# Optimization experiments

Hardware: AMD Instinct MI355X
Metric: run time of the kernel (lower is better)

## Reference

```python
import jax, jax.numpy as jnp
import numpy as np

B, T, H, DH = 4, 2048, 16, 128
D = H * DH            # inner_dim = 2048
F = 4096              # mlp_inner_dim
E = 8                 # num_expert_mlp
TOP_K = 2


def setup_inputs() -> dict:
    key = jax.random.key(0)
    ks = jax.random.split(key, 5)
    s_in = 1.0 / np.sqrt(D)
    s_f = 1.0 / np.sqrt(F)
    return {
        "stm": jax.random.normal(ks[0], (B, T, H, DH), dtype=jnp.float32),
        "gate_w": jax.random.normal(ks[1], (E, D), dtype=jnp.float32) * s_in,
        "w1": jax.random.normal(ks[2], (E, F, D), dtype=jnp.float32) * s_in,
        "w2": jax.random.normal(ks[3], (E, D, F), dtype=jnp.float32) * s_f,
        "w3": jax.random.normal(ks[4], (E, F, D), dtype=jnp.float32) * s_in,
    }


def reference(stm, gate_w, w1, w2, w3):
    b, t, h, dh = stm.shape
    d = h * dh
    x = stm.reshape(b * t, d)                                   # [N, D]
    logits = x @ gate_w.T                                       # [N, E]
    top_logit, top_idx = jax.lax.top_k(logits, TOP_K)           # [N, 2]
    gw = jax.nn.softmax(top_logit.astype(jnp.float32), axis=1).astype(x.dtype)
    out = jnp.zeros_like(x)
    n_expert = w1.shape[0]
    for e in range(n_expert):
        # combine weight for expert e per token (0 if not routed)
        we = jnp.sum(jnp.where(top_idx == e, gw, jnp.zeros_like(gw)), axis=1)  # [N]
        gate = jax.nn.silu(x @ w1[e].T)                          # [N, F]
        up = x @ w3[e].T                                         # [N, F]
        y = (gate * up) @ w2[e].T                                # [N, D]
        out = out + we[:, None] * y
    return out.reshape(b, t, h, dh)
```

## Files before the change

kernel.cpp:

```cpp
#include <hip/hip_runtime.h>
#include <hip/hip_bf16.h>
#include <stdint.h>

#define N_TOK 8192
#define DIM   2048
#define FDIM  4096
#define NEXP  8

#define XB_OFF   0ull
#define HB_OFF   33554432ull
#define WB1_OFF  176160768ull
#define WB3_OFF  243269632ull
#define META_OFF 310378496ull
#define CNT_OFF   (META_OFF)
#define EBASE_OFF (META_OFF + 64ull)
#define ELIST_OFF (META_OFF + 128ull)
#define EWTS_OFF  (ELIST_OFF + 262144ull)

typedef float f32x4 __attribute__((ext_vector_type(4)));
typedef short s16x8 __attribute__((ext_vector_type(8)));

__device__ __forceinline__ uint32_t pkbf(float a, float b) {
  uint32_t ua = __builtin_bit_cast(uint32_t, a) + 0x8000u;
  uint32_t ub = __builtin_bit_cast(uint32_t, b) + 0x8000u;
  return (ua >> 16) | (ub & 0xffff0000u);
}

__device__ __forceinline__ void gld16(const void* g, void* l) {
  __builtin_amdgcn_global_load_lds(
      (__attribute__((address_space(1))) void*)g,
      (__attribute__((address_space(3))) void*)l, 16, 0, 0);
}

__device__ __forceinline__ void conv_chunks(
    const float* __restrict__ src, __hip_bfloat16* __restrict__ dst,
    int r0, int nrh, int rtot, int kd, int idx0, int stride, int total) {
  const int cpr = kd / 8;
  for (int i = idx0; i < total; i += stride) {
    const int e = i / (nrh * cpr);
    const int rem = i - e * nrh * cpr;
    const int lr = rem / cpr;
    const int c = rem - lr * cpr;
    const float* s = src + ((size_t)e * rtot + r0 + lr) * (size_t)kd + c * 8;
    const float4 a = *(const float4*)s;
    const float4 b = *(const float4*)(s + 4);
    uint4 u;
    u.x = pkbf(a.x, a.y); u.y = pkbf(a.z, a.w);
    u.z = pkbf(b.x, b.y); u.w = pkbf(b.z, b.w);
    *(uint4*)(dst + ((size_t)e * nrh + lr) * (size_t)kd + c * 8) = u;
  }
}

__global__ void init_k(int* cnt) {
  if (threadIdx.x < NEXP) cnt[threadIdx.x] = 0;
}

__global__ void router_k(const float* __restrict__ x, const float* __restrict__ gw,
                         __hip_bfloat16* __restrict__ xb, int* __restrict__ cnt,
                         int* __restrict__ elist, float* __restrict__ ewts,
                         const float* __restrict__ w1, const float* __restrict__ w3,
                         __hip_bfloat16* __restrict__ wA, __hip_bfloat16* __restrict__ wB,
                         float* __restrict__ out) {
  const int blk = blockIdx.x;
  const int t = threadIdx.x;
  if (blk >= N_TOK) {
    const int cb = blk - N_TOK;
    if (cb < 4096) {
      conv_chunks(w1, wA, 0, 2048, FDIM, DIM, cb * 256 + t, 4096 * 256, 4194304);
    } else if (cb < 8192) {
      conv_chunks(w3, wB, 0, 2048, FDIM, DIM, (cb - 4096) * 256 + t, 4096 * 256, 4194304);
    } else {
      for (size_t i = (size_t)(cb - 8192) * 256 + t; i < 4194304; i += 512 * 256)
        *(float4*)(out + i * 4) = make_float4(0.f, 0.f, 0.f, 0.f);
    }
    return;
  }
  const int n = blk;
  const float* xr = x + (size_t)n * DIM;
  const float4 v0 = *(const float4*)(xr + t * 8);
  const float4 v1 = *(const float4*)(xr + t * 8 + 4);
  uint4 u;
  u.x = pkbf(v0.x, v0.y); u.y = pkbf(v0.z, v0.w);
  u.z = pkbf(v1.x, v1.y); u.w = pkbf(v1.z, v1.w);
  *(uint4*)(xb + (size_t)n * DIM + t * 8) = u;

  float p[NEXP];
#pragma unroll
  for (int e = 0; e < NEXP; ++e) {
    const float* g = gw + e * DIM + t * 8;
    const float4 g0 = *(const float4*)g;
    const float4 g1 = *(const float4*)(g + 4);
    p[e] = v0.x * g0.x + v0.y * g0.y + v0.z * g0.z + v0.w * g0.w +
           v1.x * g1.x + v1.y * g1.y + v1.z * g1.z + v1.w * g1.w;
  }
#pragma unroll
  for (int off = 32; off >= 1; off >>= 1)
#pragma unroll
    for (int e = 0; e < NEXP; ++e) p[e] += __shfl_xor(p[e], off, 64);

  __shared__ float red[4][NEXP];
  const int lane = t & 63, wv = t >> 6;
  if (lane == 0) {
#pragma unroll
    for (int e = 0; e < NEXP; ++e) red[wv][e] = p[e];
  }
  __syncthreads();
  if (t == 0) {
    float l0 = -1e30f, l1 = -1e30f;
    int e0 = 0, e1 = 0;
#pragma unroll
    for (int e = 0; e < NEXP; ++e) {
      float v = red[0][e] + red[1][e] + red[2][e] + red[3][e];
      if (v > l0) { l1 = l0; e1 = e0; l0 = v; e0 = e; }
      else if (v > l1) { l1 = v; e1 = e; }
    }
    const float ed = expf(l1 - l0);
    const float inv = 1.f / (1.f + ed);
    int s0 = atomicAdd(cnt + e0, 1);
    elist[e0 * N_TOK + s0] = n;
    ewts[e0 * N_TOK + s0] = inv;
    int s1 = atomicAdd(cnt + e1, 1);
    elist[e1 * N_TOK + s1] = (int)((uint32_t)n | 0x80000000u);
    ewts[e1 * N_TOK + s1] = ed * inv;
  }
}

__global__ void scan_k(const int* __restrict__ cnt, int* __restrict__ ebase) {
  if (threadIdx.x == 0 && blockIdx.x == 0) {
    int b = 0;
    for (int e = 0; e < NEXP; ++e) { ebase[e] = b; b += (cnt[e] + 127) & ~127; }
  }
}

__global__ void convH_k(const float* __restrict__ w1, __hip_bfloat16* __restrict__ d1,
                        const float* __restrict__ w3, __hip_bfloat16* __restrict__ d3,
                        int r0) {
  const int idx0 = blockIdx.x * 256 + threadIdx.x;
  conv_chunks(w1, d1, r0, 2048, FDIM, DIM, idx0, 4096 * 256, 4194304);
  conv_chunks(w3, d3, r0, 2048, FDIM, DIM, idx0, 4096 * 256, 4194304);
}

__global__ void convW_k(const float* __restrict__ src, __hip_bfloat16* __restrict__ dst,
                        int r0, int nrh, int rtot, int kd) {
  conv_chunks(src, dst, r0, nrh, rtot, kd,
              blockIdx.x * blockDim.x + threadIdx.x, gridDim.x * blockDim.x,
              NEXP * nrh * (kd / 8));
}

__global__ __launch_bounds__(256, 2) void moe_up_k(
    const __hip_bfloat16* __restrict__ xb, const __hip_bfloat16* __restrict__ w1b,
    const __hip_bfloat16* __restrict__ w3b, __hip_bfloat16* __restrict__ hb,
    const int* __restrict__ cnt, const int* __restrict__ ebase,
    const int* __restrict__ elist, int noff) {
  constexpr int NT = DIM / 32;
  const int e = blockIdx.z;
  const int count = cnt[e];
  const int mt = blockIdx.y;
  if (mt * 128 >= count) return;
  const int bn0 = blockIdx.x * 128;
  const int ncol0 = noff + bn0;

  __shared__ char lds[73728];
  const int t = threadIdx.x;
  const int lane = t & 63, wv = t >> 6;
  const int wr = wv >> 1, wc = wv & 1;
  const int* lst = elist + e * N_TOK;
  const size_t hrow0 = (size_t)ebase[e] + (size_t)mt * 128;

  const int r0 = t >> 2;
  const int ks = (t & 3) ^ ((r0 >> 1) & 3);
  size_t sA[2], sB1[2];
  int ldsO[2];
#pragma unroll
  for (int i = 0; i < 2; ++i) {
    const int r = r0 + i * 64;
    int idx = mt * 128 + r;
    if (idx >= count) idx = 0;
    const size_t tok = (size_t)(lst[idx] & 0x7fffffff);
    sA[i] = tok * DIM + ks * 8;
    sB1[i] = ((size_t)e * 2048 + bn0 + r) * DIM + ks * 8;
    ldsO[i] = i * 4096 + wv * 1024;
  }

  const int fr = lane & 15;
  const int swzc = ((lane >> 4) ^ ((fr >> 1) & 3)) << 4;
  const int aoff = (wr * 64 + fr) * 64 + swzc;
  const int boff = (wc * 64 + fr) * 64 + swzc;

  f32x4 accG[4][4], accU[4][4];
#pragma unroll
  for (int mi = 0; mi < 4; ++mi)
#pragma unroll
    for (int ni = 0; ni < 4; ++ni) {
      accG[mi][ni] = {0.f, 0.f, 0.f, 0.f};
      accU[mi][ni] = {0.f, 0.f, 0.f, 0.f};
    }

  auto stage = [&](int kt, int b) {
    const int k0 = kt * 32;
    char* base = lds + b * 24576;
#pragma unroll
    for (int i = 0; i < 2; ++i)
      gld16(xb + sA[i] + k0, base + ldsO[i]);
#pragma unroll
    for (int i = 0; i < 2; ++i)
      gld16(w1b + sB1[i] + k0, base + 8192 + ldsO[i]);
#pragma unroll
    for (int i = 0; i < 2; ++i)
      gld16(w3b + sB1[i] + k0, base + 16384 + ldsO[i]);
  };

  stage(0, 0);
  stage(1, 1);
  asm volatile("s_waitcnt vmcnt(6)" ::: "memory");
  __builtin_amdgcn_sched_barrier(0);
  __builtin_amdgcn_s_barrier();
  __builtin_amdgcn_sched_barrier(0);

  int bR = 0, bS = 2;
#pragma unroll 3
  for (int kt = 0; kt < NT; ++kt) {
    const int t2 = (kt + 2 < NT) ? kt + 2 : NT - 1;
    stage(t2, bS);
    char* base = lds + bR * 24576;
    s16x8 af[4], b1f[4], b3f[4];
#pragma unroll
    for (int mi = 0; mi < 4; ++mi)
      af[mi] = *(const s16x8*)(base + aoff + mi * 1024);
#pragma unroll
    for (int ni = 0; ni < 4; ++ni) {
      b1f[ni] = *(const s16x8*)(base + 8192 + boff + ni * 1024);
      b3f[ni] = *(const s16x8*)(base + 16384 + boff + ni * 1024);
    }
#pragma unroll
    for (int mi = 0; mi < 4; ++mi)
#pragma unroll
      for (int ni = 0; ni < 4; ++ni) {
        accG[mi][ni] = __builtin_amdgcn_mfma_f32_16x16x32_bf16(
            af[mi], b1f[ni], accG[mi][ni], 0, 0, 0);
        accU[mi][ni] = __builtin_amdgcn_mfma_f32_16x16x32_bf16(
            af[mi], b3f[ni], accU[mi][ni], 0, 0, 0);
      }
    asm volatile("s_waitcnt vmcnt(6)" ::: "memory");
    __builtin_amdgcn_sched_barrier(0);
    __builtin_amdgcn_s_barrier();
    __builtin_amdgcn_sched_barrier(0);
    bR = (bR == 2) ? 0 : bR + 1;
    bS = (bS == 2) ? 0 : bS + 1;
  }

  const int erow = (lane >> 4) * 4;
  const int ecol = lane & 15;
#pragma unroll
  for (int mi = 0; mi < 4; ++mi)
#pragma unroll
    for (int ni = 0; ni < 4; ++ni) {
      const size_t cb = ncol0 + wc * 64 + ni * 16 + ecol;
#pragma unroll
      for (int j = 0; j < 4; ++j) {
        const size_t r = hrow0 + wr * 64 + mi * 16 + erow + j;
        const float g = accG[mi][ni][j];
        const float uu = accU[mi][ni][j];
        const float h = g / (1.f + __expf(-g)) * uu;
        hb[r * FDIM + cb] = __float2bfloat16(h);
      }
    }
}

__global__ __launch_bounds__(256, 2) void moe_down_k(
    const __hip_bfloat16* __restrict__ hb, const __hip_bfloat16* __restrict__ w2b,
    float* __restrict__ out, const int* __restrict__ cnt,
    const int* __restrict__ ebase, const int* __restrict__ elist,
    const float* __restrict__ ewts) {
  constexpr int NT = FDIM / 32;
  const int e = blockIdx.z;
  const int count = cnt[e];
  const int mt = blockIdx.y;
  if (mt * 128 >= count) return;
  const int bn0 = blockIdx.x * 256;

  __shared__ char lds[73728];
  const int t = threadIdx.x;
  const int lane = t & 63, wv = t >> 6;
  const int wr = wv >> 1, wc = wv & 1;
  const int* lst = elist + e * N_TOK;
  const size_t hrow0 = (size_t)ebase[e] + (size_t)mt * 128;

  const int r0 = t >> 2;
  const int ks = (t & 3) ^ ((r0 >> 1) & 3);
  size_t sA[2], sB[2];
  int ldsO[2];
#pragma unroll
  for (int i = 0; i < 2; ++i) {
    const int r = r0 + i * 64;
    sA[i] = (hrow0 + r) * (size_t)FDIM + ks * 8;
    sB[i] = ((size_t)e * 2048 + bn0 + r) * (size_t)FDIM + ks * 8;
    ldsO[i] = i * 4096 + wv * 1024;
  }
  const size_t sBp = 128 * (size_t)FDIM;

  const int fr = lane & 15;
  const int swzc = ((lane >> 4) ^ ((fr >> 1) & 3)) << 4;
  const int aoff = (wr * 64 + fr) * 64 + swzc;
  const int boff = (wc * 64 + fr) * 64 + swzc;

  f32x4 accP[2][4][4];
#pragma unroll
  for (int p = 0; p < 2; ++p)
#pragma unroll
    for (int mi = 0; mi < 4; ++mi)
#pragma unroll
      for (int ni = 0; ni < 4; ++ni) accP[p][mi][ni] = {0.f, 0.f, 0.f, 0.f};

  auto stage = [&](int kt, int b) {
    const int k0 = kt * 32;
    char* base = lds + b * 24576;
#pragma unroll
    for (int i = 0; i < 2; ++i)
      gld16(hb + sA[i] + k0, base + ldsO[i]);
#pragma unroll
    for (int i = 0; i < 2; ++i)
      gld16(w2b + sB[i] + k0, base + 8192 + ldsO[i]);
#pragma unroll
    for (int i = 0; i < 2; ++i)
      gld16(w2b + sB[i] + sBp + k0, base + 16384 + ldsO[i]);
  };

  stage(0, 0);
  stage(1, 1);
  asm volatile("s_waitcnt vmcnt(6)" ::: "memory");
  __builtin_amdgcn_sched_barrier(0);
  __builtin_amdgcn_s_barrier();
  __builtin_amdgcn_sched_barrier(0);

  int bR = 0, bS = 2;
#pragma unroll 3
  for (int kt = 0; kt < NT; ++kt) {
    const int t2 = (kt + 2 < NT) ? kt + 2 : NT - 1;
    stage(t2, bS);
    char* base = lds + bR * 24576;
    s16x8 af[4], b0f[4], b1f[4];
#pragma unroll
    for (int mi = 0; mi < 4; ++mi)
      af[mi] = *(const s16x8*)(base + aoff + mi * 1024);
#pragma unroll
    for (int ni = 0; ni < 4; ++ni) {
      b0f[ni] = *(const s16x8*)(base + 8192 + boff + ni * 1024);
      b1f[ni] = *(const s16x8*)(base + 16384 + boff + ni * 1024);
    }
#pragma unroll
    for (int mi = 0; mi < 4; ++mi)
#pragma unroll
      for (int ni = 0; ni < 4; ++ni) {
        accP[0][mi][ni] = __builtin_amdgcn_mfma_f32_16x16x32_bf16(
            af[mi], b0f[ni], accP[0][mi][ni], 0, 0, 0);
        accP[1][mi][ni] = __builtin_amdgcn_mfma_f32_16x16x32_bf16(
            af[mi], b1f[ni], accP[1][mi][ni], 0, 0, 0);
      }
    asm volatile("s_waitcnt vmcnt(6)" ::: "memory");
    __builtin_amdgcn_sched_barrier(0);
    __builtin_amdgcn_s_barrier();
    __builtin_amdgcn_sched_barrier(0);
    bR = (bR == 2) ? 0 : bR + 1;
    bS = (bS == 2) ? 0 : bS + 1;
  }

  const int erow = (lane >> 4) * 4;
  const int ecol = lane & 15;
#pragma unroll
  for (int mi = 0; mi < 4; ++mi)
#pragma unroll
    for (int j = 0; j < 4; ++j) {
      const int i = mt * 128 + wr * 64 + mi * 16 + erow + j;
      if (i < count) {
        const uint32_t info = (uint32_t)lst[i];
        const int tok = (int)(info & 0x7fffffffu);
        const float wt = ewts[e * N_TOK + i];
        float* prow = out + (size_t)tok * DIM;
#pragma unroll
        for (int p = 0; p < 2; ++p)
#pragma unroll
          for (int ni = 0; ni < 4; ++ni) {
            const int cb = bn0 + p * 128 + wc * 64 + ni * 16 + ecol;
            atomicAdd(prow + cb, wt * accP[p][mi][ni][j]);
          }
      }
    }
}

extern "C" void kernel_launch(void* const* d_in, const int* in_sizes, int n_in,
                              void* d_out, int out_size, void* d_ws, size_t ws_size,
                              hipStream_t stream) {
  const float* stm = (const float*)d_in[0];
  const float* gw = (const float*)d_in[1];
  const float* w1 = (const float*)d_in[2];
  const float* w2 = (const float*)d_in[3];
  const float* w3 = (const float*)d_in[4];
  float* out = (float*)d_out;
  char* ws = (char*)d_ws;

  __hip_bfloat16* xb = (__hip_bfloat16*)(ws + XB_OFF);
  __hip_bfloat16* hb = (__hip_bfloat16*)(ws + HB_OFF);
  __hip_bfloat16* wb1 = (__hip_bfloat16*)(ws + WB1_OFF);
  __hip_bfloat16* wb3 = (__hip_bfloat16*)(ws + WB3_OFF);
  __hip_bfloat16* w2full = (__hip_bfloat16*)(ws + WB1_OFF);
  int* cnt = (int*)(ws + CNT_OFF);
  int* ebase = (int*)(ws + EBASE_OFF);
  int* elist = (int*)(ws + ELIST_OFF);
  float* ewts = (float*)(ws + EWTS_OFF);

  init_k<<<1, 64, 0, stream>>>(cnt);
  router_k<<<N_TOK + 8704, 256, 0, stream>>>(stm, gw, xb, cnt, elist, ewts,
                                             w1, w3, wb1, wb3, out);
  scan_k<<<1, 64, 0, stream>>>(cnt, ebase);

  const dim3 gUp(16, 64, 8);
  const dim3 gDn(8, 64, 8);

  moe_up_k<<<gUp, 256, 0, stream>>>(xb, wb1, wb3, hb, cnt, ebase, elist, 0);

  convH_k<<<4096, 256, 0, stream>>>(w1, wb1, w3, wb3, 2048);
  moe_up_k<<<gUp, 256, 0, stream>>>(xb, wb1, wb3, hb, cnt, ebase, elist, 2048);

  convW_k<<<4096, 256, 0, stream>>>(w2, w2full, 0, 2048, DIM, FDIM);
  moe_down_k<<<gDn, 256, 0, stream>>>(hb, w2full, out, cnt, ebase, elist, ewts);
}
```

Before: 1.350 ms.

## Enlarge MoE GEMM tiles to 256 rows with 512-thread, 8-wave blocks

Both expert GEMM kernels move from 256-thread blocks with 128-row M tiles to 512-thread blocks with 256-row M tiles. Expert segments are padded to 256 rows to match. In the up kernel the 8 waves share one B tile, and the down kernel now uses a 4x2 wave grid over a 256x256 output tile with 8x4 accumulators per wave. The aim is to halve weight re-reads per token and raise arithmetic intensity. The cost is fewer resident blocks, more padding waste per expert and higher register pressure in the down kernel.

Result: slower. 1.408 ms (+4.3%).

```diff
diff --git a/kernel.cpp b/kernel.cpp
--- a/kernel.cpp
+++ b/kernel.cpp
@@ -128,7 +128,7 @@
 __global__ void scan_k(const int* __restrict__ cnt, int* __restrict__ ebase) {
   if (threadIdx.x == 0 && blockIdx.x == 0) {
     int b = 0;
-    for (int e = 0; e < NEXP; ++e) { ebase[e] = b; b += (cnt[e] + 127) & ~127; }
+    for (int e = 0; e < NEXP; ++e) { ebase[e] = b; b += (cnt[e] + 255) & ~255; }
   }
 }
 
@@ -147,7 +147,7 @@
               NEXP * nrh * (kd / 8));
 }
 
-__global__ __launch_bounds__(256, 2) void moe_up_k(
+__global__ __launch_bounds__(512, 1) void moe_up_k(
     const __hip_bfloat16* __restrict__ xb, const __hip_bfloat16* __restrict__ w1b,
     const __hip_bfloat16* __restrict__ w3b, __hip_bfloat16* __restrict__ hb,
     const int* __restrict__ cnt, const int* __restrict__ ebase,
@@ -156,36 +156,39 @@
   const int e = blockIdx.z;
   const int count = cnt[e];
   const int mt = blockIdx.y;
-  if (mt * 128 >= count) return;
+  if (mt * 256 >= count) return;
   const int bn0 = blockIdx.x * 128;
   const int ncol0 = noff + bn0;
 
-  __shared__ char lds[73728];
+  __shared__ char lds[98304];
   const int t = threadIdx.x;
   const int lane = t & 63, wv = t >> 6;
   const int wr = wv >> 1, wc = wv & 1;
   const int* lst = elist + e * N_TOK;
-  const size_t hrow0 = (size_t)ebase[e] + (size_t)mt * 128;
-
-  const int r0 = t >> 2;
-  const int ks = (t & 3) ^ ((r0 >> 1) & 3);
-  size_t sA[2], sB1[2];
-  int ldsO[2];
+  const size_t hrow0 = (size_t)ebase[e] + (size_t)mt * 256;
+
+  const int sl = t & 3;
+  size_t sA[2];
+  int ldsA[2];
 #pragma unroll
   for (int i = 0; i < 2; ++i) {
-    const int r = r0 + i * 64;
-    int idx = mt * 128 + r;
+    const int row = (t >> 2) + i * 128;
+    const int gsrc = sl ^ ((row >> 1) & 3);
+    int idx = mt * 256 + row;
     if (idx >= count) idx = 0;
     const size_t tok = (size_t)(lst[idx] & 0x7fffffff);
-    sA[i] = tok * DIM + ks * 8;
-    sB1[i] = ((size_t)e * 2048 + bn0 + r) * DIM + ks * 8;
-    ldsO[i] = i * 4096 + wv * 1024;
-  }
+    sA[i] = tok * DIM + gsrc * 8;
+    ldsA[i] = wv * 1024 + i * 8192;
+  }
+  const int rB = t >> 2;
+  const int gsrcB = sl ^ ((rB >> 1) & 3);
+  const size_t sB = ((size_t)e * 2048 + bn0 + rB) * DIM + gsrcB * 8;
+  const int ldsB = 16384 + wv * 1024;
 
   const int fr = lane & 15;
   const int swzc = ((lane >> 4) ^ ((fr >> 1) & 3)) << 4;
   const int aoff = (wr * 64 + fr) * 64 + swzc;
-  const int boff = (wc * 64 + fr) * 64 + swzc;
+  const int boff = 16384 + (wc * 64 + fr) * 64 + swzc;
 
   f32x4 accG[4][4], accU[4][4];
 #pragma unroll
@@ -198,21 +201,17 @@
 
   auto stage = [&](int kt, int b) {
     const int k0 = kt * 32;
-    char* base = lds + b * 24576;
+    char* base = lds + b * 32768;
 #pragma unroll
     for (int i = 0; i < 2; ++i)
-      gld16(xb + sA[i] + k0, base + ldsO[i]);
-#pragma unroll
-    for (int i = 0; i < 2; ++i)
-      gld16(w1b + sB1[i] + k0, base + 8192 + ldsO[i]);
-#pragma unroll
-    for (int i = 0; i < 2; ++i)
-      gld16(w3b + sB1[i] + k0, base + 16384 + ldsO[i]);
+      gld16(xb + sA[i] + k0, base + ldsA[i]);
+    gld16(w1b + sB + k0, base + ldsB);
+    gld16(w3b + sB + k0, base + ldsB + 8192);
   };
 
   stage(0, 0);
   stage(1, 1);
-  asm volatile("s_waitcnt vmcnt(6)" ::: "memory");
+  asm volatile("s_waitcnt vmcnt(4)" ::: "memory");
   __builtin_amdgcn_sched_barrier(0);
   __builtin_amdgcn_s_barrier();
   __builtin_amdgcn_sched_barrier(0);
@@ -222,15 +221,15 @@
   for (int kt = 0; kt < NT; ++kt) {
     const int t2 = (kt + 2 < NT) ? kt + 2 : NT - 1;
     stage(t2, bS);
-    char* base = lds + bR * 24576;
+    char* base = lds + bR * 32768;
     s16x8 af[4], b1f[4], b3f[4];
 #pragma unroll
     for (int mi = 0; mi < 4; ++mi)
       af[mi] = *(const s16x8*)(base + aoff + mi * 1024);
 #pragma unroll
     for (int ni = 0; ni < 4; ++ni) {
-      b1f[ni] = *(const s16x8*)(base + 8192 + boff + ni * 1024);
-      b3f[ni] = *(const s16x8*)(base + 16384 + boff + ni * 1024);
+      b1f[ni] = *(const s16x8*)(base + boff + ni * 1024);
+      b3f[ni] = *(const s16x8*)(base + boff + 8192 + ni * 1024);
     }
 #pragma unroll
     for (int mi = 0; mi < 4; ++mi)
@@ -241,7 +240,7 @@
         accU[mi][ni] = __builtin_amdgcn_mfma_f32_16x16x32_bf16(
             af[mi], b3f[ni], accU[mi][ni], 0, 0, 0);
       }
-    asm volatile("s_waitcnt vmcnt(6)" ::: "memory");
+    asm volatile("s_waitcnt vmcnt(4)" ::: "memory");
     __builtin_amdgcn_sched_barrier(0);
     __builtin_amdgcn_s_barrier();
     __builtin_amdgcn_sched_barrier(0);
@@ -267,7 +266,7 @@
     }
 }
 
-__global__ __launch_bounds__(256, 2) void moe_down_k(
+__global__ __launch_bounds__(512, 1) void moe_down_k(
     const __hip_bfloat16* __restrict__ hb, const __hip_bfloat16* __restrict__ w2b,
     float* __restrict__ out, const int* __restrict__ cnt,
     const int* __restrict__ ebase, const int* __restrict__ elist,
@@ -276,59 +275,53 @@
   const int e = blockIdx.z;
   const int count = cnt[e];
   const int mt = blockIdx.y;
-  if (mt * 128 >= count) return;
+  if (mt * 256 >= count) return;
   const int bn0 = blockIdx.x * 256;
 
-  __shared__ char lds[73728];
+  __shared__ char lds[98304];
   const int t = threadIdx.x;
   const int lane = t & 63, wv = t >> 6;
-  const int wr = wv >> 1, wc = wv & 1;
+  const int wr = wv >> 2, wc = wv & 3;
   const int* lst = elist + e * N_TOK;
-  const size_t hrow0 = (size_t)ebase[e] + (size_t)mt * 128;
-
-  const int r0 = t >> 2;
-  const int ks = (t & 3) ^ ((r0 >> 1) & 3);
+  const size_t hrow0 = (size_t)ebase[e] + (size_t)mt * 256;
+
+  const int sl = t & 3;
   size_t sA[2], sB[2];
   int ldsO[2];
 #pragma unroll
   for (int i = 0; i < 2; ++i) {
-    const int r = r0 + i * 64;
-    sA[i] = (hrow0 + r) * (size_t)FDIM + ks * 8;
-    sB[i] = ((size_t)e * 2048 + bn0 + r) * (size_t)FDIM + ks * 8;
-    ldsO[i] = i * 4096 + wv * 1024;
-  }
-  const size_t sBp = 128 * (size_t)FDIM;
+    const int row = (t >> 2) + i * 128;
+    const int gsrc = sl ^ ((row >> 1) & 3);
+    sA[i] = (hrow0 + row) * (size_t)FDIM + gsrc * 8;
+    sB[i] = ((size_t)e * 2048 + bn0 + row) * (size_t)FDIM + gsrc * 8;
+    ldsO[i] = wv * 1024 + i * 8192;
+  }
 
   const int fr = lane & 15;
   const int swzc = ((lane >> 4) ^ ((fr >> 1) & 3)) << 4;
-  const int aoff = (wr * 64 + fr) * 64 + swzc;
-  const int boff = (wc * 64 + fr) * 64 + swzc;
-
-  f32x4 accP[2][4][4];
-#pragma unroll
-  for (int p = 0; p < 2; ++p)
-#pragma unroll
-    for (int mi = 0; mi < 4; ++mi)
-#pragma unroll
-      for (int ni = 0; ni < 4; ++ni) accP[p][mi][ni] = {0.f, 0.f, 0.f, 0.f};
+  const int aoff = (wr * 128 + fr) * 64 + swzc;
+  const int boff = 16384 + (wc * 64 + fr) * 64 + swzc;
+
+  f32x4 acc[8][4];
+#pragma unroll
+  for (int mi = 0; mi < 8; ++mi)
+#pragma unroll
+    for (int ni = 0; ni < 4; ++ni) acc[mi][ni] = {0.f, 0.f, 0.f, 0.f};
 
   auto stage = [&](int kt, int b) {
     const int k0 = kt * 32;
-    char* base = lds + b * 24576;
+    char* base = lds + b * 32768;
 #pragma unroll
     for (int i = 0; i < 2; ++i)
       gld16(hb + sA[i] + k0, base + ldsO[i]);
 #pragma unroll
     for (int i = 0; i < 2; ++i)
-      gld16(w2b + sB[i] + k0, base + 8192 + ldsO[i]);
-#pragma unroll
-    for (int i = 0; i < 2; ++i)
-      gld16(w2b + sB[i] + sBp + k0, base + 16384 + ldsO[i]);
+      gld16(w2b + sB[i] + k0, base + 16384 + ldsO[i]);
   };
 
   stage(0, 0);
   stage(1, 1);
-  asm volatile("s_waitcnt vmcnt(6)" ::: "memory");
+  asm volatile("s_waitcnt vmcnt(4)" ::: "memory");
   __builtin_amdgcn_sched_barrier(0);
   __builtin_amdgcn_s_barrier();
   __builtin_amdgcn_sched_barrier(0);
@@ -338,26 +331,21 @@
   for (int kt = 0; kt < NT; ++kt) {
     const int t2 = (kt + 2 < NT) ? kt + 2 : NT - 1;
     stage(t2, bS);
-    char* base = lds + bR * 24576;
-    s16x8 af[4], b0f[4], b1f[4];
-#pragma unroll
-    for (int mi = 0; mi < 4; ++mi)
+    char* base = lds + bR * 32768;
+    s16x8 af[8], bf[4];
+#pragma unroll
+    for (int mi = 0; mi < 8; ++mi)
       af[mi] = *(const s16x8*)(base + aoff + mi * 1024);
 #pragma unroll
-    for (int ni = 0; ni < 4; ++ni) {
-      b0f[ni] = *(const s16x8*)(base + 8192 + boff + ni * 1024);
-      b1f[ni] = *(const s16x8*)(base + 16384 + boff + ni * 1024);
-    }
-#pragma unroll
-    for (int mi = 0; mi < 4; ++mi)
-#pragma unroll
-      for (int ni = 0; ni < 4; ++ni) {
-        accP[0][mi][ni] = __builtin_amdgcn_mfma_f32_16x16x32_bf16(
-            af[mi], b0f[ni], accP[0][mi][ni], 0, 0, 0);
-        accP[1][mi][ni] = __builtin_amdgcn_mfma_f32_16x16x32_bf16(
-            af[mi], b1f[ni], accP[1][mi][ni], 0, 0, 0);
-      }
-    asm volatile("s_waitcnt vmcnt(6)" ::: "memory");
+    for (int ni = 0; ni < 4; ++ni)
+      bf[ni] = *(const s16x8*)(base + boff + ni * 1024);
+#pragma unroll
+    for (int mi = 0; mi < 8; ++mi)
+#pragma unroll
+      for (int ni = 0; ni < 4; ++ni)
+        acc[mi][ni] = __builtin_amdgcn_mfma_f32_16x16x32_bf16(
+            af[mi], bf[ni], acc[mi][ni], 0, 0, 0);
+    asm volatile("s_waitcnt vmcnt(4)" ::: "memory");
     __builtin_amdgcn_sched_barrier(0);
     __builtin_amdgcn_s_barrier();
     __builtin_amdgcn_sched_barrier(0);
@@ -368,22 +356,20 @@
   const int erow = (lane >> 4) * 4;
   const int ecol = lane & 15;
 #pragma unroll
-  for (int mi = 0; mi < 4; ++mi)
+  for (int mi = 0; mi < 8; ++mi)
 #pragma unroll
     for (int j = 0; j < 4; ++j) {
-      const int i = mt * 128 + wr * 64 + mi * 16 + erow + j;
+      const int i = mt * 256 + wr * 128 + mi * 16 + erow + j;
       if (i < count) {
         const uint32_t info = (uint32_t)lst[i];
         const int tok = (int)(info & 0x7fffffffu);
         const float wt = ewts[e * N_TOK + i];
         float* prow = out + (size_t)tok * DIM;
 #pragma unroll
-        for (int p = 0; p < 2; ++p)
-#pragma unroll
-          for (int ni = 0; ni < 4; ++ni) {
-            const int cb = bn0 + p * 128 + wc * 64 + ni * 16 + ecol;
-            atomicAdd(prow + cb, wt * accP[p][mi][ni][j]);
-          }
+        for (int ni = 0; ni < 4; ++ni) {
+          const int cb = bn0 + wc * 64 + ni * 16 + ecol;
+          atomicAdd(prow + cb, wt * acc[mi][ni][j]);
+        }
       }
     }
 }
@@ -414,14 +400,14 @@
                                              w1, w3, wb1, wb3, out);
   scan_k<<<1, 64, 0, stream>>>(cnt, ebase);
 
-  const dim3 gUp(16, 64, 8);
-  const dim3 gDn(8, 64, 8);
-
-  moe_up_k<<<gUp, 256, 0, stream>>>(xb, wb1, wb3, hb, cnt, ebase, elist, 0);
+  const dim3 gUp(16, 32, 8);
+  const dim3 gDn(8, 32, 8);
+
+  moe_up_k<<<gUp, 512, 0, stream>>>(xb, wb1, wb3, hb, cnt, ebase, elist, 0);
 
   convH_k<<<4096, 256, 0, stream>>>(w1, wb1, w3, wb3, 2048);
-  moe_up_k<<<gUp, 256, 0, stream>>>(xb, wb1, wb3, hb, cnt, ebase, elist, 2048);
+  moe_up_k<<<gUp, 512, 0, stream>>>(xb, wb1, wb3, hb, cnt, ebase, elist, 2048);
 
   convW_k<<<4096, 256, 0, stream>>>(w2, w2full, 0, 2048, DIM, FDIM);
-  moe_down_k<<<gDn, 256, 0, stream>>>(hb, w2full, out, cnt, ebase, elist, ewts);
-}
+  moe_down_k<<<gDn, 512, 0, stream>>>(hb, w2full, out, cnt, ebase, elist, ewts);
+}
```
